# Optimization experiments

Hardware: AMD Instinct MI355X
Metric: run time of the kernel (lower is better)

Reference implementation:

```python
import jax, jax.numpy as jnp
import numpy as np

EMBD = 768
FFN_HID = 2048
HEAD_DIM = 64
KV_H = 5
KV_DIM = KV_H * HEAD_DIM
Q_H = 15
EPS = 1.1920929e-07  # torch.finfo(float32).eps, nn.RMSNorm default when eps=None
MAX_WAVELENGTH = 10000.0


def rmsnorm(x, w):
    var = jnp.mean(x * x, axis=-1, keepdims=True)
    return x * jax.lax.rsqrt(var + EPS) * w


def apply_rope(q, L):
    # q: [B, L, H, D]; rotate-half RoPE applied only to queries (as in source)
    d_half = HEAD_DIM // 2
    ts = MAX_WAVELENGTH ** (2.0 / HEAD_DIM * jnp.arange(d_half, dtype=jnp.float32))
    pos = jnp.arange(L, dtype=jnp.float32)
    radians = pos[:, None] / ts[None, :]            # [L, d_half]
    s = jnp.sin(radians)[None, :, None, :]          # [1, L, 1, d_half]
    c = jnp.cos(radians)[None, :, None, :]
    q1, q2 = q[..., :d_half], q[..., d_half:]
    return jnp.concatenate([q1 * c - q2 * s, q2 * c + q1 * s], axis=-1)


def setup_inputs() -> dict:
    key = jax.random.key(0)
    ks = jax.random.split(key, 12)
    B, L, Lc = 4, 512, 2048
    sc = 0.02
    return {
        "x": jax.random.normal(ks[0], (B, L, EMBD), jnp.float32),
        "text_k": jax.random.normal(ks[1], (B, Lc, KV_DIM), jnp.float32),
        "text_v": jax.random.normal(ks[2], (B, Lc, KV_DIM), jnp.float32),
        "ln1_w": jnp.ones((EMBD,), jnp.float32),
        "ln2_w": jnp.ones((EMBD,), jnp.float32),
        "wq": jax.random.normal(ks[3], (EMBD, Q_H * HEAD_DIM), jnp.float32) * sc,
        "wk": jax.random.normal(ks[4], (KV_DIM, KV_DIM), jnp.float32) * sc,
        "wv": jax.random.normal(ks[5], (KV_DIM, KV_DIM), jnp.float32) * sc,
        "wo": jax.random.normal(ks[6], (Q_H * HEAD_DIM, EMBD), jnp.float32) * sc,
        "w_gate": jax.random.normal(ks[7], (EMBD, FFN_HID), jnp.float32) * sc,
        "w_up": jax.random.normal(ks[8], (EMBD, FFN_HID), jnp.float32) * sc,
        "w_down": jax.random.normal(ks[9], (FFN_HID, EMBD), jnp.float32) * sc,
    }


def reference(x, text_k, text_v, ln1_w, ln2_w, wq, wk, wv, wo, w_gate, w_up, w_down):
    B, L, _ = x.shape
    Lc = text_k.shape[1]

    residual = x
    x_norm = rmsnorm(x, ln1_w)
    q = (x_norm @ wq).reshape(B, L, Q_H, HEAD_DIM)
    k = (text_k @ wk).reshape(B, Lc, KV_H, HEAD_DIM)
    v = (text_v @ wv).reshape(B, Lc, KV_H, HEAD_DIM)

    q = apply_rope(q, L)

    # GQA: each of the 15 query heads maps to one of 5 kv heads
    kv_map = (jnp.arange(Q_H) * KV_H) // Q_H        # [0,0,0,1,1,1,...,4,4,4]
    k_sel = k[:, :, kv_map, :]                       # [B, Lc, Q_H, D]
    v_sel = v[:, :, kv_map, :]

    scores = jnp.einsum("blhd,bmhd->bhlm", q, k_sel) / (HEAD_DIM ** 0.5)
    attn = jax.nn.softmax(scores, axis=-1)
    ctx = jnp.einsum("bhlm,bmhd->blhd", attn, v_sel).reshape(B, L, Q_H * HEAD_DIM)

    x = ctx @ wo + residual

    residual = x
    xn = rmsnorm(x, ln2_w)
    h = jax.nn.silu(xn @ w_gate) * (xn @ w_up)       # SwiGLU
    return h @ w_down + residual
```

## Files before the change

kernel.cpp:

```cpp
#include <hip/hip_runtime.h>
#include <hip/hip_bf16.h>
#include <math.h>

#define EMBD 768
#define FFN_HID 2048
#define HEAD_DIM 64
#define KV_H 5
#define KV_DIM 320
#define Q_H 15
#define QDIM (Q_H * HEAD_DIM)
#define BB 4
#define LL 512
#define LC 2048
#define EPSV 1.1920929e-07f
#define NSP 8

typedef __attribute__((ext_vector_type(8))) __bf16 bf16x8;
typedef __attribute__((ext_vector_type(2))) __bf16 bf16x2;
typedef __attribute__((ext_vector_type(8))) short short8;
typedef __attribute__((ext_vector_type(4))) float floatx4;
typedef __attribute__((ext_vector_type(2))) unsigned uint2v;
typedef unsigned short ushort;

#define RSCALE 0.18033688011112042f

__device__ inline ushort f2bf(float f) {
  union { float f; unsigned u; } c; c.f = f;
  return (ushort)((c.u + 0x8000u) >> 16);
}
__device__ inline float bf2f(ushort s) {
  union { unsigned u; float f; } c; c.u = ((unsigned)s) << 16;
  return c.f;
}
#if __has_builtin(__builtin_amdgcn_cvt_pk_bf16_f32)
__device__ inline unsigned pk2bf(float a, float b) {
  union { bf16x2 v; unsigned u; } c;
  c.v = __builtin_amdgcn_cvt_pk_bf16_f32(a, b);
  return c.u;
}
#else
__device__ inline unsigned pk2bf(float a, float b) {
  union { float f; unsigned u; } x, y; x.f = a; y.f = b;
  return ((x.u + 0x8000u) >> 16) | ((y.u + 0x8000u) & 0xffff0000u);
}
#endif

__device__ __forceinline__ void glds16(const ushort* g, ushort* l) {
  __builtin_amdgcn_global_load_lds(
      (const __attribute__((address_space(1))) unsigned int*)g,
      (__attribute__((address_space(3))) unsigned int*)l, 16, 0, 0);
}

__global__ __launch_bounds__(256) void rmsnorm_kernel(const float* __restrict__ x,
                                                      const float* __restrict__ w,
                                                      ushort* __restrict__ out) {
  int row = blockIdx.x;
  const float* xr = x + (size_t)row * EMBD;
  ushort* orow = out + (size_t)row * EMBD;
  int tid = threadIdx.x;
  float ss = 0.f;
  for (int i = tid; i < EMBD; i += 256) { float v = xr[i]; ss += v * v; }
  for (int off = 32; off > 0; off >>= 1) ss += __shfl_down(ss, off, 64);
  __shared__ float sred[4];
  if ((tid & 63) == 0) sred[tid >> 6] = ss;
  __syncthreads();
  float tot = sred[0] + sred[1] + sred[2] + sred[3];
  float scale = rsqrtf(tot * (1.0f / EMBD) + EPSV);
  for (int i = tid; i < EMBD; i += 256) orow[i] = f2bf(xr[i] * scale * w[i]);
}

struct MD { const void* src; void* dst; const float* aux; int K; int N; int nx; int base; int mode; };
struct MD10 { MD d[10]; };

__global__ __launch_bounds__(256) void mega_prep(MD10 ds) {
  int bid = blockIdx.x;
  int sel = 0;
#pragma unroll
  for (int j = 1; j < 10; ++j) sel = (bid >= ds.d[j].base) ? j : sel;
  MD t = ds.d[sel];
  int rel = bid - t.base;
  int tid = threadIdx.x;
  if (t.mode == 1) {
    int i = rel * 256 + tid;
    float4 f = *(const float4*)((const float*)t.src + (size_t)i * 4);
    ushort* o = (ushort*)t.dst + (size_t)i * 4;
    o[0] = f2bf(f.x); o[1] = f2bf(f.y); o[2] = f2bf(f.z); o[3] = f2bf(f.w);
    return;
  }
  if (t.mode == 2) {
    const float* xr = (const float*)t.src + (size_t)rel * EMBD;
    ushort* orow = (ushort*)t.dst + (size_t)rel * EMBD;
    float ss = 0.f;
    for (int i = tid; i < EMBD; i += 256) { float v = xr[i]; ss += v * v; }
    for (int off = 32; off > 0; off >>= 1) ss += __shfl_down(ss, off, 64);
    __shared__ float sred[4];
    if ((tid & 63) == 0) sred[tid >> 6] = ss;
    __syncthreads();
    float tot = sred[0] + sred[1] + sred[2] + sred[3];
    float scale = rsqrtf(tot * (1.0f / EMBD) + EPSV);
    for (int i = tid; i < EMBD; i += 256) orow[i] = f2bf(xr[i] * scale * t.aux[i]);
    return;
  }
  int bx = rel % t.nx, by = rel / t.nx;
  int k0 = by * 64, n0 = bx * 64;
  __shared__ ushort T[64][72];
  int r = tid >> 2, cb = (tid & 3) * 16;
#pragma unroll
  for (int i = 0; i < 16; i += 4) {
    float4 f = *(const float4*)((const float*)t.src + (size_t)(k0 + r) * t.N + n0 + cb + i);
    T[r][cb + i + 0] = f2bf(f.x); T[r][cb + i + 1] = f2bf(f.y);
    T[r][cb + i + 2] = f2bf(f.z); T[r][cb + i + 3] = f2bf(f.w);
  }
  __syncthreads();
#pragma unroll
  for (int i = 0; i < 2; ++i) {
    short8 v;
#pragma unroll
    for (int j = 0; j < 8; ++j) v[j] = (short)T[cb + i * 8 + j][r];
    *(short8*)((ushort*)t.dst + (size_t)(n0 + r) * t.K + k0 + cb + i * 8) = v;
  }
}

__global__ __launch_bounds__(256) void gemm128r(const ushort* __restrict__ A,
                                                const ushort* __restrict__ Bt,
                                                const float* __restrict__ Rf,
                                                float* __restrict__ Cout,
                                                int M, int N, int K) {
  __shared__ ushort As[2][128 * 64];
  __shared__ ushort Bs[2][64 * 64];
  int tid = threadIdx.x;
  int w = tid >> 6, lane = tid & 63;
  int lm = lane & 15, lq = lane >> 4;
  int m0 = blockIdx.y * 128, n0 = blockIdx.x * 64;
  int wm = (w & 1) * 64, wn = (w >> 1) * 32;
  int arow = lane >> 3, acol = ((lane & 7) ^ arow) << 3;
  int kg[2] = {((lq) ^ (lm & 7)) << 3, ((4 + lq) ^ (lm & 7)) << 3};
  floatx4 acc[4][2];
#pragma unroll
  for (int i = 0; i < 4; ++i)
#pragma unroll
    for (int j = 0; j < 2; ++j) acc[i][j] = (floatx4){0.f, 0.f, 0.f, 0.f};
  for (int k0 = 0; k0 < K; k0 += 128) {
    int two = (k0 + 64 < K) ? 1 : 0;
#pragma unroll 2
    for (int c = 0; c <= two; ++c) {
      int kk = k0 + c * 64;
#pragma unroll
      for (int s = 0; s < 4; ++s) {
        int g = (w << 2) + s;
        glds16(A + (size_t)(m0 + g * 8 + arow) * K + kk + acol, &As[c][g * 512]);
      }
#pragma unroll
      for (int s = 0; s < 2; ++s) {
        int g = (w << 1) + s;
        glds16(Bt + (size_t)(n0 + g * 8 + arow) * K + kk + acol, &Bs[c][g * 512]);
      }
    }
    __syncthreads();
#pragma unroll 2
    for (int c = 0; c <= two; ++c) {
#pragma unroll
      for (int kc = 0; kc < 2; ++kc) {
        bf16x8 af[4], bf[2];
#pragma unroll
        for (int mt = 0; mt < 4; ++mt)
          af[mt] = *(const bf16x8*)&As[c][(wm + mt * 16 + lm) * 64 + kg[kc]];
#pragma unroll
        for (int nt = 0; nt < 2; ++nt)
          bf[nt] = *(const bf16x8*)&Bs[c][(wn + nt * 16 + lm) * 64 + kg[kc]];
#pragma unroll
        for (int mt = 0; mt < 4; ++mt)
#pragma unroll
          for (int nt = 0; nt < 2; ++nt)
            acc[mt][nt] = __builtin_amdgcn_mfma_f32_16x16x32_bf16(af[mt], bf[nt], acc[mt][nt], 0, 0, 0);
      }
    }
    __syncthreads();
  }
#pragma unroll
  for (int mt = 0; mt < 4; ++mt)
#pragma unroll
    for (int nt = 0; nt < 2; ++nt)
#pragma unroll
      for (int r = 0; r < 4; ++r) {
        int row = m0 + wm + mt * 16 + lq * 4 + r;
        int col = n0 + wn + nt * 16 + lm;
        size_t idx = (size_t)row * N + col;
        Cout[idx] = acc[mt][nt][r] + Rf[idx];
      }
}

__global__ __launch_bounds__(256) void gemm_kv128(const ushort* __restrict__ Ak,
                                                  const ushort* __restrict__ Av,
                                                  const ushort* __restrict__ Btk,
                                                  const ushort* __restrict__ Btv,
                                                  ushort* __restrict__ Ck,
                                                  ushort* __restrict__ Vt,
                                                  int M, int N, int K) {
  const ushort* A = blockIdx.z ? Av : Ak;
  const ushort* Bt = blockIdx.z ? Btv : Btk;
  __shared__ ushort As[128 * 64];
  __shared__ ushort Bs[64 * 64];
  int tid = threadIdx.x;
  int w = tid >> 6, lane = tid & 63;
  int lm = lane & 15, lq = lane >> 4;
  int m0 = blockIdx.y * 128, n0 = blockIdx.x * 64;
  int wm = (w & 1) * 64, wn = (w >> 1) * 32;
  int arow = lane >> 3, acol = ((lane & 7) ^ arow) << 3;
  int kg[2] = {((lq) ^ (lm & 7)) << 3, ((4 + lq) ^ (lm & 7)) << 3};
  floatx4 acc[4][2];
#pragma unroll
  for (int i = 0; i < 4; ++i)
#pragma unroll
    for (int j = 0; j < 2; ++j) acc[i][j] = (floatx4){0.f, 0.f, 0.f, 0.f};
  for (int k0 = 0; k0 < K; k0 += 64) {
#pragma unroll
    for (int s = 0; s < 4; ++s) {
      int g = (w << 2) + s;
      glds16(A + (size_t)(m0 + g * 8 + arow) * K + k0 + acol, &As[g * 512]);
    }
#pragma unroll
    for (int s = 0; s < 2; ++s) {
      int g = (w << 1) + s;
      glds16(Bt + (size_t)(n0 + g * 8 + arow) * K + k0 + acol, &Bs[g * 512]);
    }
    __syncthreads();
#pragma unroll
    for (int kc = 0; kc < 2; ++kc) {
      bf16x8 af[4], bf[2];
#pragma unroll
      for (int mt = 0; mt < 4; ++mt)
        af[mt] = *(const bf16x8*)&As[(wm + mt * 16 + lm) * 64 + kg[kc]];
#pragma unroll
      for (int nt = 0; nt < 2; ++nt)
        bf[nt] = *(const bf16x8*)&Bs[(wn + nt * 16 + lm) * 64 + kg[kc]];
#pragma unroll
      for (int mt = 0; mt < 4; ++mt)
#pragma unroll
        for (int nt = 0; nt < 2; ++nt)
          acc[mt][nt] = __builtin_amdgcn_mfma_f32_16x16x32_bf16(af[mt], bf[nt], acc[mt][nt], 0, 0, 0);
    }
    __syncthreads();
  }
  if (blockIdx.z == 0) {
#pragma unroll
    for (int mt = 0; mt < 4; ++mt)
#pragma unroll
      for (int nt = 0; nt < 2; ++nt)
#pragma unroll
        for (int r = 0; r < 4; ++r) {
          int row = m0 + wm + mt * 16 + lq * 4 + r;
          int col = n0 + wn + nt * 16 + lm;
          Ck[(size_t)row * N + col] = f2bf(acc[mt][nt][r]);
        }
  } else {
    int kvh = n0 >> 6;
#pragma unroll
    for (int mt = 0; mt < 4; ++mt)
#pragma unroll
      for (int nt = 0; nt < 2; ++nt) {
        int d = wn + nt * 16 + lm;
        int grow = m0 + wm + mt * 16 + lq * 4;
        int b = grow >> 11;
        int tok = grow & (LC - 1);
        size_t a = ((size_t)(b * KV_H + kvh) * 64 + d) * LC + tok;
        uint2v pk = (uint2v){pk2bf(acc[mt][nt][0], acc[mt][nt][1]),
                             pk2bf(acc[mt][nt][2], acc[mt][nt][3])};
        *(uint2v*)&Vt[a] = pk;
      }
  }
}

__global__ __launch_bounds__(256) void gemm_q_rope(const ushort* __restrict__ A,
                                                   const ushort* __restrict__ Bt,
                                                   ushort* __restrict__ Q,
                                                   int M, int N, int K) {
  __shared__ ushort As[128 * 64];
  __shared__ ushort Bs[64 * 64];
  int tid = threadIdx.x;
  int w = tid >> 6, lane = tid & 63;
  int lm = lane & 15, lq = lane >> 4;
  int m0 = blockIdx.y * 128, n0 = blockIdx.x * 64;
  int wm = (w & 1) * 64, wn = (w >> 1) * 16;
  int arow = lane >> 3, acol = ((lane & 7) ^ arow) << 3;
  int kg[2] = {((lq) ^ (lm & 7)) << 3, ((4 + lq) ^ (lm & 7)) << 3};
  floatx4 acc[4][2];
#pragma unroll
  for (int i = 0; i < 4; ++i)
#pragma unroll
    for (int j = 0; j < 2; ++j) acc[i][j] = (floatx4){0.f, 0.f, 0.f, 0.f};
  for (int k0 = 0; k0 < K; k0 += 64) {
#pragma unroll
    for (int s = 0; s < 4; ++s) {
      int g = (w << 2) + s;
      glds16(A + (size_t)(m0 + g * 8 + arow) * K + k0 + acol, &As[g * 512]);
    }
#pragma unroll
    for (int s = 0; s < 2; ++s) {
      int g = (w << 1) + s;
      glds16(Bt + (size_t)(n0 + g * 8 + arow) * K + k0 + acol, &Bs[g * 512]);
    }
    __syncthreads();
#pragma unroll
    for (int kc = 0; kc < 2; ++kc) {
      bf16x8 af[4], bf[2];
#pragma unroll
      for (int mt = 0; mt < 4; ++mt)
        af[mt] = *(const bf16x8*)&As[(wm + mt * 16 + lm) * 64 + kg[kc]];
#pragma unroll
      for (int nt = 0; nt < 2; ++nt) {
        int br = wn + nt * 32 + lm;
        bf[nt] = *(const bf16x8*)&Bs[br * 64 + (((kc * 4 + lq) ^ (br & 7)) << 3)];
      }
#pragma unroll
      for (int mt = 0; mt < 4; ++mt)
#pragma unroll
        for (int nt = 0; nt < 2; ++nt)
          acc[mt][nt] = __builtin_amdgcn_mfma_f32_16x16x32_bf16(af[mt], bf[nt], acc[mt][nt], 0, 0, 0);
    }
    __syncthreads();
  }
  int d = wn + lm;
  float invts = exp2f(-(float)d * 0.4152410118609203f);
#pragma unroll
  for (int mt = 0; mt < 4; ++mt)
#pragma unroll
    for (int r = 0; r < 4; ++r) {
      int row = m0 + wm + mt * 16 + lq * 4 + r;
      int l = row & (LL - 1);
      float th = (float)l * invts;
      float s, c;
      __sincosf(th, &s, &c);
      float q1 = acc[mt][0][r], q2 = acc[mt][1][r];
      size_t base = (size_t)row * N + n0 + d;
      Q[base] = f2bf((q1 * c - q2 * s) * RSCALE);
      Q[base + 32] = f2bf((q2 * c + q1 * s) * RSCALE);
    }
}

__global__ __launch_bounds__(256) void gemm_gateup(const ushort* __restrict__ A,
                                                   const ushort* __restrict__ Bg,
                                                   const ushort* __restrict__ Bu,
                                                   ushort* __restrict__ H,
                                                   int M, int N, int K) {
  __shared__ ushort As[128 * 64];
  __shared__ ushort Bs0[64 * 64];
  __shared__ ushort Bs1[64 * 64];
  int tid = threadIdx.x;
  int w = tid >> 6, lane = tid & 63;
  int lm = lane & 15, lq = lane >> 4;
  int m0 = blockIdx.y * 128, n0 = blockIdx.x * 64;
  int wm = (w & 1) * 64, wn = (w >> 1) * 32;
  int arow = lane >> 3, acol = ((lane & 7) ^ arow) << 3;
  int kg[2] = {((lq) ^ (lm & 7)) << 3, ((4 + lq) ^ (lm & 7)) << 3};
  floatx4 accg[4][2], accu[4][2];
#pragma unroll
  for (int i = 0; i < 4; ++i)
#pragma unroll
    for (int j = 0; j < 2; ++j) {
      accg[i][j] = (floatx4){0.f, 0.f, 0.f, 0.f};
      accu[i][j] = (floatx4){0.f, 0.f, 0.f, 0.f};
    }
  for (int k0 = 0; k0 < K; k0 += 64) {
#pragma unroll
    for (int s = 0; s < 4; ++s) {
      int g = (w << 2) + s;
      glds16(A + (size_t)(m0 + g * 8 + arow) * K + k0 + acol, &As[g * 512]);
    }
#pragma unroll
    for (int s = 0; s < 2; ++s) {
      int g = (w << 1) + s;
      glds16(Bg + (size_t)(n0 + g * 8 + arow) * K + k0 + acol, &Bs0[g * 512]);
      glds16(Bu + (size_t)(n0 + g * 8 + arow) * K + k0 + acol, &Bs1[g * 512]);
    }
    __syncthreads();
#pragma unroll
    for (int kc = 0; kc < 2; ++kc) {
      bf16x8 af[4], bg[2], bu[2];
#pragma unroll
      for (int mt = 0; mt < 4; ++mt)
        af[mt] = *(const bf16x8*)&As[(wm + mt * 16 + lm) * 64 + kg[kc]];
#pragma unroll
      for (int nt = 0; nt < 2; ++nt) {
        bg[nt] = *(const bf16x8*)&Bs0[(wn + nt * 16 + lm) * 64 + kg[kc]];
        bu[nt] = *(const bf16x8*)&Bs1[(wn + nt * 16 + lm) * 64 + kg[kc]];
      }
#pragma unroll
      for (int mt = 0; mt < 4; ++mt)
#pragma unroll
        for (int nt = 0; nt < 2; ++nt) {
          accg[mt][nt] = __builtin_amdgcn_mfma_f32_16x16x32_bf16(af[mt], bg[nt], accg[mt][nt], 0, 0, 0);
          accu[mt][nt] = __builtin_amdgcn_mfma_f32_16x16x32_bf16(af[mt], bu[nt], accu[mt][nt], 0, 0, 0);
        }
    }
    __syncthreads();
  }
#pragma unroll
  for (int mt = 0; mt < 4; ++mt)
#pragma unroll
    for (int nt = 0; nt < 2; ++nt)
#pragma unroll
      for (int r = 0; r < 4; ++r) {
        int row = m0 + wm + mt * 16 + lq * 4 + r;
        int col = n0 + wn + nt * 16 + lm;
        float gv = accg[mt][nt][r];
        float hv = gv / (1.f + __expf(-gv)) * accu[mt][nt][r];
        H[(size_t)row * N + col] = f2bf(hv);
      }
}

__global__ __launch_bounds__(256) void attn_kernel(const ushort* __restrict__ qb,
                                                   const ushort* __restrict__ kb,
                                                   const ushort* __restrict__ vt,
                                                   ushort* __restrict__ Op,
                                                   float* __restrict__ Ml) {
  int bid = blockIdx.x;
  int sp = bid & 7;
  int qt = (bid >> 3) & 3;
  int g = bid >> 5;
  int b = g / 15, h = g - b * 15;
  int kvh = h / 3;
  int l0 = qt * 128;
  int kv0 = sp * 256;
  __shared__ ushort Ks[64 * 64];
  __shared__ ushort Vs[64 * 64];
  __shared__ ushort Ps[4][32][72];
  ushort* Qs = &Ps[0][0][0];
  int tid = threadIdx.x;
  int w = tid >> 6, lane = tid & 63, lm = lane & 15, lq = lane >> 4;
  int arow = lane >> 3, acol = ((lane & 7) ^ arow) << 3;
  int kg[2] = {((lq) ^ (lm & 7)) << 3, ((4 + lq) ^ (lm & 7)) << 3};
  const ushort* kbase = kb + (size_t)b * LC * KV_DIM + kvh * HEAD_DIM;
  const ushort* vbase = vt + (size_t)(b * KV_H + kvh) * 64 * LC;
#pragma unroll
  for (int s = 0; s < 4; ++s) {
    int gg = (w << 2) + s;
    glds16(qb + (size_t)(b * LL + l0 + gg * 8 + arow) * QDIM + h * HEAD_DIM + acol, &Qs[gg * 512]);
  }
  __syncthreads();
  bf16x8 aq[2][2];
#pragma unroll
  for (int q2 = 0; q2 < 2; ++q2) {
    int qr = w * 32 + q2 * 16 + lm;
    aq[q2][0] = *(const bf16x8*)&Qs[qr * 64 + kg[0]];
    aq[q2][1] = *(const bf16x8*)&Qs[qr * 64 + kg[1]];
  }
  bf16x8 bones;
  {
    short8 o = {0x3F80, 0x3F80, 0x3F80, 0x3F80, 0x3F80, 0x3F80, 0x3F80, 0x3F80};
    bones = *(bf16x8*)&o;
  }
  floatx4 oacc[4][2];
#pragma unroll
  for (int i = 0; i < 4; ++i)
#pragma unroll
    for (int j = 0; j < 2; ++j) oacc[i][j] = (floatx4){0.f, 0.f, 0.f, 0.f};
  floatx4 lacc[2] = {(floatx4){0.f, 0.f, 0.f, 0.f}, (floatx4){0.f, 0.f, 0.f, 0.f}};

  for (int t = 0; t < 4; ++t) {
    int m0 = kv0 + t * 64;
#pragma unroll
    for (int s = 0; s < 2; ++s) {
      int gg = (w << 1) + s;
      glds16(kbase + (size_t)(m0 + gg * 8 + arow) * KV_DIM + acol, &Ks[gg * 512]);
      glds16(vbase + (size_t)(gg * 8 + arow) * LC + m0 + acol, &Vs[gg * 512]);
    }
    __syncthreads();

    floatx4 sacc[4][2];
#pragma unroll
    for (int nt = 0; nt < 4; ++nt)
#pragma unroll
      for (int q2 = 0; q2 < 2; ++q2) sacc[nt][q2] = (floatx4){0.f, 0.f, 0.f, 0.f};
#pragma unroll
    for (int kc = 0; kc < 2; ++kc) {
#pragma unroll
      for (int nt = 0; nt < 4; ++nt) {
        bf16x8 bk = *(const bf16x8*)&Ks[(nt * 16 + lm) * 64 + kg[kc]];
#pragma unroll
        for (int q2 = 0; q2 < 2; ++q2)
          sacc[nt][q2] = __builtin_amdgcn_mfma_f32_16x16x32_bf16(bk, aq[q2][kc], sacc[nt][q2], 0, 0, 0);
      }
    }
#pragma unroll
    for (int nt = 0; nt < 4; ++nt)
#pragma unroll
      for (int q2 = 0; q2 < 2; ++q2) {
        float p0 = exp2f(sacc[nt][q2][0]);
        float p1 = exp2f(sacc[nt][q2][1]);
        float p2 = exp2f(sacc[nt][q2][2]);
        float p3 = exp2f(sacc[nt][q2][3]);
        uint2v pk = (uint2v){pk2bf(p0, p1), pk2bf(p2, p3)};
        *(uint2v*)&Ps[w][q2 * 16 + lm][nt * 16 + lq * 4] = pk;
      }
#pragma unroll
    for (int kc2 = 0; kc2 < 2; ++kc2) {
      bf16x8 ap[2];
      ap[0] = *(const bf16x8*)&Ps[w][lm][kc2 * 32 + lq * 8];
      ap[1] = *(const bf16x8*)&Ps[w][16 + lm][kc2 * 32 + lq * 8];
#pragma unroll
      for (int dt = 0; dt < 4; ++dt) {
        bf16x8 bv = *(const bf16x8*)&Vs[(dt * 16 + lm) * 64 + kg[kc2]];
#pragma unroll
        for (int q2 = 0; q2 < 2; ++q2)
          oacc[dt][q2] = __builtin_amdgcn_mfma_f32_16x16x32_bf16(ap[q2], bv, oacc[dt][q2], 0, 0, 0);
      }
      lacc[0] = __builtin_amdgcn_mfma_f32_16x16x32_bf16(ap[0], bones, lacc[0], 0, 0, 0);
      lacc[1] = __builtin_amdgcn_mfma_f32_16x16x32_bf16(ap[1], bones, lacc[1], 0, 0, 0);
    }
    __syncthreads();
  }
#pragma unroll
  for (int q2 = 0; q2 < 2; ++q2)
#pragma unroll
    for (int r = 0; r < 4; ++r) {
      int row = l0 + w * 32 + q2 * 16 + lq * 4 + r;
      size_t base = ((size_t)sp * (BB * LL) + b * LL + row) * QDIM + h * HEAD_DIM;
#pragma unroll
      for (int dt = 0; dt < 4; ++dt) Op[base + dt * 16 + lm] = f2bf(oacc[dt][q2][r]);
      if (lm == 0) Ml[((size_t)sp * (BB * LL) + b * LL + row) * Q_H + h] = lacc[q2][r];
    }
}

__global__ __launch_bounds__(256) void combine_kernel(ushort* __restrict__ Op,
                                                      const float* __restrict__ Ml,
                                                      ushort* __restrict__ ctx) {
  int t = threadIdx.x;
  int half = t >> 7;
  int t2 = t & 127;
  if (t2 >= 120) return;
  int bl = blockIdx.x * 2 + half;
  int h = t2 >> 3;
  float lsum = 0.f;
#pragma unroll
  for (int s = 0; s < NSP; ++s) lsum += Ml[((size_t)s * (BB * LL) + bl) * Q_H + h];
  float inv = 1.f / lsum;
  size_t i0 = (size_t)bl * QDIM + t2 * 8;
  float o[8] = {0.f, 0.f, 0.f, 0.f, 0.f, 0.f, 0.f, 0.f};
#pragma unroll
  for (int s = 0; s < NSP; ++s) {
    short8 v = *(const short8*)(Op + (size_t)s * (BB * LL) * QDIM + i0);
#pragma unroll
    for (int j = 0; j < 8; ++j) o[j] += bf2f((ushort)v[j]);
  }
  short8 r;
#pragma unroll
  for (int j = 0; j < 8; ++j) r[j] = (short)f2bf(o[j] * inv);
  *(short8*)(ctx + i0) = r;
}

extern "C" void kernel_launch(void* const* d_in, const int* in_sizes, int n_in,
                              void* d_out, int out_size, void* d_ws, size_t ws_size,
                              hipStream_t stream) {
  const float* x      = (const float*)d_in[0];
  const float* text_k = (const float*)d_in[1];
  const float* text_v = (const float*)d_in[2];
  const float* ln1_w  = (const float*)d_in[3];
  const float* ln2_w  = (const float*)d_in[4];
  const float* wq     = (const float*)d_in[5];
  const float* wk     = (const float*)d_in[6];
  const float* wv     = (const float*)d_in[7];
  const float* wo     = (const float*)d_in[8];
  const float* w_gate = (const float*)d_in[9];
  const float* w_up   = (const float*)d_in[10];
  const float* w_down = (const float*)d_in[11];
  float* out = (float*)d_out;
  char* base = (char*)d_ws;

  const int BL = BB * LL;
  const int BLC = BB * LC;

  ushort* xnorm = (ushort*)(base + 0);
  ushort* wqt   = (ushort*)(base + 3145728);
  ushort* wkt   = (ushort*)(base + 4620288);
  ushort* wvt   = (ushort*)(base + 4825088);
  ushort* wot   = (ushort*)(base + 5029888);
  ushort* wgt   = (ushort*)(base + 6504448);
  ushort* wut   = (ushort*)(base + 9650176);
  ushort* wdt   = (ushort*)(base + 12795904);
  ushort* kbuf  = (ushort*)(base + 15941632);
  ushort* vtb   = (ushort*)(base + 21184512);
  float*  x2    = (float*) (base + 26427392);
  ushort* qb    = (ushort*)(base + 32718848);
  ushort* tkb   = (ushort*)(base + 36651008);
  ushort* tvb   = (ushort*)(base + 41893888);
  float*  Ml    = (float*) (base + 47136768);
  char* SCR = base + 48119808;
  ushort* Op    = (ushort*)SCR;
  ushort* ctxb  = (ushort*)SCR;
  ushort* gbuf  = (ushort*)(base + 15941632);

  MD10 ds;
  const int NKV4 = BLC * KV_DIM / 1024;
  ds.d[0] = {wq,     wqt,   nullptr, EMBD,    QDIM,    QDIM / 64,    0,    0};
  ds.d[1] = {wk,     wkt,   nullptr, KV_DIM,  KV_DIM,  KV_DIM / 64,  180,  0};
  ds.d[2] = {wv,     wvt,   nullptr, KV_DIM,  KV_DIM,  KV_DIM / 64,  205,  0};
  ds.d[3] = {wo,     wot,   nullptr, QDIM,    EMBD,    EMBD / 64,    230,  0};
  ds.d[4] = {w_gate, wgt,   nullptr, EMBD,    FFN_HID, FFN_HID / 64, 410,  0};
  ds.d[5] = {w_up,   wut,   nullptr, EMBD,    FFN_HID, FFN_HID / 64, 794,  0};
  ds.d[6] = {w_down, wdt,   nullptr, FFN_HID, EMBD,    EMBD / 64,    1178, 0};
  ds.d[7] = {text_k, tkb,   nullptr, 0, 0, 0, 1562, 1};
  ds.d[8] = {text_v, tvb,   nullptr, 0, 0, 0, 1562 + NKV4, 1};
  ds.d[9] = {x,      xnorm, ln1_w,   0, 0, 0, 1562 + 2 * NKV4, 2};
  const int nmega = 1562 + 2 * NKV4 + BL;
  mega_prep<<<nmega, 256, 0, stream>>>(ds);

  gemm_kv128<<<dim3(KV_DIM / 64, BLC / 128, 2), 256, 0, stream>>>(tkb, tvb, wkt, wvt, kbuf, vtb, BLC, KV_DIM, KV_DIM);

  gemm_q_rope<<<dim3(QDIM / 64, BL / 128), 256, 0, stream>>>(xnorm, wqt, qb, BL, QDIM, EMBD);

  attn_kernel<<<1920, 256, 0, stream>>>(qb, kbuf, vtb, Op, Ml);
  combine_kernel<<<BL / 2, 256, 0, stream>>>(Op, Ml, ctxb);

  gemm128r<<<dim3(EMBD / 64, BL / 128), 256, 0, stream>>>(ctxb, wot, x, x2, BL, EMBD, QDIM);

  rmsnorm_kernel<<<BL, 256, 0, stream>>>(x2, ln2_w, xnorm);
  gemm_gateup<<<dim3(FFN_HID / 64, BL / 128), 256, 0, stream>>>(xnorm, wgt, wut, gbuf, BL, FFN_HID, EMBD);
  gemm128r<<<dim3(EMBD / 64, BL / 128), 256, 0, stream>>>(gbuf, wdt, x2, out, BL, EMBD, FFN_HID);
}
```

Measured before the change: 146.8 us.

## Fuse text K/V bf16 conversion into projection GEMM and merge with Q GEMM

Removes the fp32->bf16 conversion pass for text_k/text_v from the prep kernel. The KV GEMM now reads fp32 activations directly, converts them in registers and stores them swizzled into shared memory. The KV and Q-with-RoPE GEMMs are merged into one launch of 880 blocks. This drops a full round trip of the bf16 text buffers through memory and one kernel launch. In exchange, the A-tile load becomes synchronous register loads instead of direct global-to-LDS copies, which may reduce latency hiding.

```diff
diff --git a/kernel.cpp b/kernel.cpp
--- a/kernel.cpp
+++ b/kernel.cpp
@@ -20,6 +20,7 @@
 typedef __attribute__((ext_vector_type(8))) short short8;
 typedef __attribute__((ext_vector_type(4))) float floatx4;
 typedef __attribute__((ext_vector_type(2))) unsigned uint2v;
+typedef __attribute__((ext_vector_type(4))) unsigned uint4v;
 typedef unsigned short ushort;
 
 #define RSCALE 0.18033688011112042f
@@ -80,13 +81,6 @@
   MD t = ds.d[sel];
   int rel = bid - t.base;
   int tid = threadIdx.x;
-  if (t.mode == 1) {
-    int i = rel * 256 + tid;
-    float4 f = *(const float4*)((const float*)t.src + (size_t)i * 4);
-    ushort* o = (ushort*)t.dst + (size_t)i * 4;
-    o[0] = f2bf(f.x); o[1] = f2bf(f.y); o[2] = f2bf(f.z); o[3] = f2bf(f.w);
-    return;
-  }
   if (t.mode == 2) {
     const float* xr = (const float*)t.src + (size_t)rel * EMBD;
     ushort* orow = (ushort*)t.dst + (size_t)rel * EMBD;
@@ -190,115 +184,120 @@
       }
 }
 
-__global__ __launch_bounds__(256) void gemm_kv128(const ushort* __restrict__ Ak,
-                                                  const ushort* __restrict__ Av,
+__global__ __launch_bounds__(256) void kvq_kernel(const float* __restrict__ tk,
+                                                  const float* __restrict__ tv,
                                                   const ushort* __restrict__ Btk,
                                                   const ushort* __restrict__ Btv,
+                                                  const ushort* __restrict__ xnorm,
+                                                  const ushort* __restrict__ wqt,
                                                   ushort* __restrict__ Ck,
                                                   ushort* __restrict__ Vt,
-                                                  int M, int N, int K) {
-  const ushort* A = blockIdx.z ? Av : Ak;
-  const ushort* Bt = blockIdx.z ? Btv : Btk;
+                                                  ushort* __restrict__ Q) {
   __shared__ ushort As[128 * 64];
   __shared__ ushort Bs[64 * 64];
+  int bid = blockIdx.x;
   int tid = threadIdx.x;
   int w = tid >> 6, lane = tid & 63;
   int lm = lane & 15, lq = lane >> 4;
-  int m0 = blockIdx.y * 128, n0 = blockIdx.x * 64;
-  int wm = (w & 1) * 64, wn = (w >> 1) * 32;
   int arow = lane >> 3, acol = ((lane & 7) ^ arow) << 3;
   int kg[2] = {((lq) ^ (lm & 7)) << 3, ((4 + lq) ^ (lm & 7)) << 3};
+
+  if (bid < 640) {
+    int bz = bid / 320;
+    int rem = bid - bz * 320;
+    int bx = rem % 5, by = rem / 5;
+    const float* Af = bz ? tv : tk;
+    const ushort* Bt = bz ? Btv : Btk;
+    int m0 = by * 128, n0 = bx * 64;
+    int wm = (w & 1) * 64, wn = (w >> 1) * 32;
+    floatx4 acc[4][2];
+#pragma unroll
+    for (int i = 0; i < 4; ++i)
+#pragma unroll
+      for (int j = 0; j < 2; ++j) acc[i][j] = (floatx4){0.f, 0.f, 0.f, 0.f};
+    for (int k0 = 0; k0 < KV_DIM; k0 += 64) {
+#pragma unroll
+      for (int s = 0; s < 4; ++s) {
+        int rr = ((w << 2) + s) * 8 + arow;
+        const float* src = Af + (size_t)(m0 + rr) * KV_DIM + k0 + ((lane & 7) << 3);
+        float4 a0 = *(const float4*)src;
+        float4 a1 = *(const float4*)(src + 4);
+        uint4v pv = (uint4v){pk2bf(a0.x, a0.y), pk2bf(a0.z, a0.w),
+                             pk2bf(a1.x, a1.y), pk2bf(a1.z, a1.w)};
+        *(uint4v*)&As[rr * 64 + (((lane & 7) ^ arow) << 3)] = pv;
+      }
+#pragma unroll
+      for (int s = 0; s < 2; ++s) {
+        int g = (w << 1) + s;
+        glds16(Bt + (size_t)(n0 + g * 8 + arow) * KV_DIM + k0 + acol, &Bs[g * 512]);
+      }
+      __syncthreads();
+#pragma unroll
+      for (int kc = 0; kc < 2; ++kc) {
+        bf16x8 af[4], bf[2];
+#pragma unroll
+        for (int mt = 0; mt < 4; ++mt)
+          af[mt] = *(const bf16x8*)&As[(wm + mt * 16 + lm) * 64 + kg[kc]];
+#pragma unroll
+        for (int nt = 0; nt < 2; ++nt)
+          bf[nt] = *(const bf16x8*)&Bs[(wn + nt * 16 + lm) * 64 + kg[kc]];
+#pragma unroll
+        for (int mt = 0; mt < 4; ++mt)
+#pragma unroll
+          for (int nt = 0; nt < 2; ++nt)
+            acc[mt][nt] = __builtin_amdgcn_mfma_f32_16x16x32_bf16(af[mt], bf[nt], acc[mt][nt], 0, 0, 0);
+      }
+      __syncthreads();
+    }
+    if (bz == 0) {
+#pragma unroll
+      for (int mt = 0; mt < 4; ++mt)
+#pragma unroll
+        for (int nt = 0; nt < 2; ++nt)
+#pragma unroll
+          for (int r = 0; r < 4; ++r) {
+            int row = m0 + wm + mt * 16 + lq * 4 + r;
+            int col = n0 + wn + nt * 16 + lm;
+            Ck[(size_t)row * KV_DIM + col] = f2bf(acc[mt][nt][r]);
+          }
+    } else {
+      int kvh = bx;
+#pragma unroll
+      for (int mt = 0; mt < 4; ++mt)
+#pragma unroll
+        for (int nt = 0; nt < 2; ++nt) {
+          int d = wn + nt * 16 + lm;
+          int grow = m0 + wm + mt * 16 + lq * 4;
+          int b = grow >> 11;
+          int tok = grow & (LC - 1);
+          size_t a = ((size_t)(b * KV_H + kvh) * 64 + d) * LC + tok;
+          uint2v pk = (uint2v){pk2bf(acc[mt][nt][0], acc[mt][nt][1]),
+                               pk2bf(acc[mt][nt][2], acc[mt][nt][3])};
+          *(uint2v*)&Vt[a] = pk;
+        }
+    }
+    return;
+  }
+
+  int r0 = bid - 640;
+  int bx = r0 % 15, by = r0 / 15;
+  int m0 = by * 128, n0 = bx * 64;
+  int wm = (w & 1) * 64, wn = (w >> 1) * 16;
   floatx4 acc[4][2];
 #pragma unroll
   for (int i = 0; i < 4; ++i)
 #pragma unroll
     for (int j = 0; j < 2; ++j) acc[i][j] = (floatx4){0.f, 0.f, 0.f, 0.f};
-  for (int k0 = 0; k0 < K; k0 += 64) {
+  for (int k0 = 0; k0 < EMBD; k0 += 64) {
 #pragma unroll
     for (int s = 0; s < 4; ++s) {
       int g = (w << 2) + s;
-      glds16(A + (size_t)(m0 + g * 8 + arow) * K + k0 + acol, &As[g * 512]);
+      glds16(xnorm + (size_t)(m0 + g * 8 + arow) * EMBD + k0 + acol, &As[g * 512]);
     }
 #pragma unroll
     for (int s = 0; s < 2; ++s) {
       int g = (w << 1) + s;
-      glds16(Bt + (size_t)(n0 + g * 8 + arow) * K + k0 + acol, &Bs[g * 512]);
-    }
-    __syncthreads();
-#pragma unroll
-    for (int kc = 0; kc < 2; ++kc) {
-      bf16x8 af[4], bf[2];
-#pragma unroll
-      for (int mt = 0; mt < 4; ++mt)
-        af[mt] = *(const bf16x8*)&As[(wm + mt * 16 + lm) * 64 + kg[kc]];
-#pragma unroll
-      for (int nt = 0; nt < 2; ++nt)
-        bf[nt] = *(const bf16x8*)&Bs[(wn + nt * 16 + lm) * 64 + kg[kc]];
-#pragma unroll
-      for (int mt = 0; mt < 4; ++mt)
-#pragma unroll
-        for (int nt = 0; nt < 2; ++nt)
-          acc[mt][nt] = __builtin_amdgcn_mfma_f32_16x16x32_bf16(af[mt], bf[nt], acc[mt][nt], 0, 0, 0);
-    }
-    __syncthreads();
-  }
-  if (blockIdx.z == 0) {
-#pragma unroll
-    for (int mt = 0; mt < 4; ++mt)
-#pragma unroll
-      for (int nt = 0; nt < 2; ++nt)
-#pragma unroll
-        for (int r = 0; r < 4; ++r) {
-          int row = m0 + wm + mt * 16 + lq * 4 + r;
-          int col = n0 + wn + nt * 16 + lm;
-          Ck[(size_t)row * N + col] = f2bf(acc[mt][nt][r]);
-        }
-  } else {
-    int kvh = n0 >> 6;
-#pragma unroll
-    for (int mt = 0; mt < 4; ++mt)
-#pragma unroll
-      for (int nt = 0; nt < 2; ++nt) {
-        int d = wn + nt * 16 + lm;
-        int grow = m0 + wm + mt * 16 + lq * 4;
-        int b = grow >> 11;
-        int tok = grow & (LC - 1);
-        size_t a = ((size_t)(b * KV_H + kvh) * 64 + d) * LC + tok;
-        uint2v pk = (uint2v){pk2bf(acc[mt][nt][0], acc[mt][nt][1]),
-                             pk2bf(acc[mt][nt][2], acc[mt][nt][3])};
-        *(uint2v*)&Vt[a] = pk;
-      }
-  }
-}
-
-__global__ __launch_bounds__(256) void gemm_q_rope(const ushort* __restrict__ A,
-                                                   const ushort* __restrict__ Bt,
-                                                   ushort* __restrict__ Q,
-                                                   int M, int N, int K) {
-  __shared__ ushort As[128 * 64];
-  __shared__ ushort Bs[64 * 64];
-  int tid = threadIdx.x;
-  int w = tid >> 6, lane = tid & 63;
-  int lm = lane & 15, lq = lane >> 4;
-  int m0 = blockIdx.y * 128, n0 = blockIdx.x * 64;
-  int wm = (w & 1) * 64, wn = (w >> 1) * 16;
-  int arow = lane >> 3, acol = ((lane & 7) ^ arow) << 3;
-  int kg[2] = {((lq) ^ (lm & 7)) << 3, ((4 + lq) ^ (lm & 7)) << 3};
-  floatx4 acc[4][2];
-#pragma unroll
-  for (int i = 0; i < 4; ++i)
-#pragma unroll
-    for (int j = 0; j < 2; ++j) acc[i][j] = (floatx4){0.f, 0.f, 0.f, 0.f};
-  for (int k0 = 0; k0 < K; k0 += 64) {
-#pragma unroll
-    for (int s = 0; s < 4; ++s) {
-      int g = (w << 2) + s;
-      glds16(A + (size_t)(m0 + g * 8 + arow) * K + k0 + acol, &As[g * 512]);
-    }
-#pragma unroll
-    for (int s = 0; s < 2; ++s) {
-      int g = (w << 1) + s;
-      glds16(Bt + (size_t)(n0 + g * 8 + arow) * K + k0 + acol, &Bs[g * 512]);
+      glds16(wqt + (size_t)(n0 + g * 8 + arow) * EMBD + k0 + acol, &Bs[g * 512]);
     }
     __syncthreads();
 #pragma unroll
@@ -332,7 +331,7 @@
       float s, c;
       __sincosf(th, &s, &c);
       float q1 = acc[mt][0][r], q2 = acc[mt][1][r];
-      size_t base = (size_t)row * N + n0 + d;
+      size_t base = (size_t)row * QDIM + n0 + d;
       Q[base] = f2bf((q1 * c - q2 * s) * RSCALE);
       Q[base + 32] = f2bf((q2 * c + q1 * s) * RSCALE);
     }
@@ -568,7 +567,6 @@
   char* base = (char*)d_ws;
 
   const int BL = BB * LL;
-  const int BLC = BB * LC;
 
   ushort* xnorm = (ushort*)(base + 0);
   ushort* wqt   = (ushort*)(base + 3145728);
@@ -582,8 +580,6 @@
   ushort* vtb   = (ushort*)(base + 21184512);
   float*  x2    = (float*) (base + 26427392);
   ushort* qb    = (ushort*)(base + 32718848);
-  ushort* tkb   = (ushort*)(base + 36651008);
-  ushort* tvb   = (ushort*)(base + 41893888);
   float*  Ml    = (float*) (base + 47136768);
   char* SCR = base + 48119808;
   ushort* Op    = (ushort*)SCR;
@@ -591,7 +587,6 @@
   ushort* gbuf  = (ushort*)(base + 15941632);
 
   MD10 ds;
-  const int NKV4 = BLC * KV_DIM / 1024;
   ds.d[0] = {wq,     wqt,   nullptr, EMBD,    QDIM,    QDIM / 64,    0,    0};
   ds.d[1] = {wk,     wkt,   nullptr, KV_DIM,  KV_DIM,  KV_DIM / 64,  180,  0};
   ds.d[2] = {wv,     wvt,   nullptr, KV_DIM,  KV_DIM,  KV_DIM / 64,  205,  0};
@@ -599,15 +594,13 @@
   ds.d[4] = {w_gate, wgt,   nullptr, EMBD,    FFN_HID, FFN_HID / 64, 410,  0};
   ds.d[5] = {w_up,   wut,   nullptr, EMBD,    FFN_HID, FFN_HID / 64, 794,  0};
   ds.d[6] = {w_down, wdt,   nullptr, FFN_HID, EMBD,    EMBD / 64,    1178, 0};
-  ds.d[7] = {text_k, tkb,   nullptr, 0, 0, 0, 1562, 1};
-  ds.d[8] = {text_v, tvb,   nullptr, 0, 0, 0, 1562 + NKV4, 1};
-  ds.d[9] = {x,      xnorm, ln1_w,   0, 0, 0, 1562 + 2 * NKV4, 2};
-  const int nmega = 1562 + 2 * NKV4 + BL;
+  ds.d[7] = {x,      xnorm, ln1_w,   0, 0, 0, 1562, 2};
+  ds.d[8] = {x,      xnorm, ln1_w,   0, 0, 0, 0x7fffffff, 2};
+  ds.d[9] = {x,      xnorm, ln1_w,   0, 0, 0, 0x7fffffff, 2};
+  const int nmega = 1562 + BL;
   mega_prep<<<nmega, 256, 0, stream>>>(ds);
 
-  gemm_kv128<<<dim3(KV_DIM / 64, BLC / 128, 2), 256, 0, stream>>>(tkb, tvb, wkt, wvt, kbuf, vtb, BLC, KV_DIM, KV_DIM);
-
-  gemm_q_rope<<<dim3(QDIM / 64, BL / 128), 256, 0, stream>>>(xnorm, wqt, qb, BL, QDIM, EMBD);
+  kvq_kernel<<<880, 256, 0, stream>>>(text_k, text_v, wkt, wvt, xnorm, wqt, kbuf, vtb, qb);
 
   attn_kernel<<<1920, 256, 0, stream>>>(qb, kbuf, vtb, Op, Ml);
   combine_kernel<<<BL / 2, 256, 0, stream>>>(Op, Ml, ctxb);
```

Result: faster. 143.3 us, median of 2 (-2.4%).
